# Kernel tuning notes

Hardware: AMD Instinct MI355X
Metric: run time of the kernel (lower is better)

## Reference

```python
import jax, jax.numpy as jnp
import numpy as np

B, N, D = 2, 2048, 768
H = 12
HD = D // H
HID = 4 * D
SCALE = HD ** -0.5
EPS = 1e-5


def layer_norm(x, g, b):
    mu = jnp.mean(x, axis=-1, keepdims=True)
    var = jnp.var(x, axis=-1, keepdims=True)
    return (x - mu) * jax.lax.rsqrt(var + EPS) * g + b


def setup_inputs() -> dict:
    key = jax.random.key(0)
    ks = jax.random.split(key, 12)
    s = 0.02
    return {
        "x": jax.random.normal(ks[0], (B, N, D), jnp.float32),
        "att_mask": jax.random.randint(ks[1], (B, N), 0, 2, jnp.int32),
        "ln1_g": jnp.ones((D,), jnp.float32),
        "ln1_b": jnp.zeros((D,), jnp.float32),
        "qkv_w": jax.random.normal(ks[2], (3 * D, D), jnp.float32) * s,
        "q_bias": jnp.zeros((D,), jnp.float32),
        "v_bias": jnp.zeros((D,), jnp.float32),
        "proj_w": jax.random.normal(ks[3], (D, D), jnp.float32) * s,
        "proj_b": jnp.zeros((D,), jnp.float32),
        "ln2_g": jnp.ones((D,), jnp.float32),
        "ln2_b": jnp.zeros((D,), jnp.float32),
        "fc1_w": jax.random.normal(ks[4], (HID, D), jnp.float32) * s,
        "fc1_b": jnp.zeros((HID,), jnp.float32),
        "fc2_w": jax.random.normal(ks[5], (D, HID), jnp.float32) * s,
        "fc2_b": jnp.zeros((D,), jnp.float32),
        "gamma_1": 0.1 * jnp.ones((D,), jnp.float32),
        "gamma_2": 0.1 * jnp.ones((D,), jnp.float32),
    }


def reference(x, att_mask, ln1_g, ln1_b, qkv_w, q_bias, v_bias, proj_w, proj_b,
              ln2_g, ln2_b, fc1_w, fc1_b, fc2_w, fc2_b, gamma_1, gamma_2):
    # --- attention branch ---
    h = layer_norm(x, ln1_g, ln1_b)
    qkv_bias = jnp.concatenate([q_bias, jnp.zeros_like(v_bias), v_bias])
    qkv = h @ qkv_w.T + qkv_bias                      # [B,N,3D]
    qkv = qkv.reshape(B, N, 3, H, HD).transpose(2, 0, 3, 1, 4)
    q, k, v = qkv[0], qkv[1], qkv[2]                  # [B,H,N,HD]
    logit = jnp.einsum('bhqd,bhkd->bhqk', q * SCALE, k)
    mask = att_mask[:, None, None, :]                 # key mask [B,1,1,N]
    logit = jnp.where(mask == 0, -jnp.inf, logit)
    attn = jax.nn.softmax(logit, axis=-1)
    o = jnp.einsum('bhqk,bhkd->bhqd', attn, v)
    o = o.transpose(0, 2, 1, 3).reshape(B, N, D)
    o = o @ proj_w.T + proj_b
    x = x + gamma_1 * o
    # --- mlp branch ---
    h2 = layer_norm(x, ln2_g, ln2_b)
    h2 = jax.nn.gelu(h2 @ fc1_w.T + fc1_b, approximate=False)
    h2 = h2 @ fc2_w.T + fc2_b
    return x + gamma_2 * h2
```

## Files before the change

kernel.cpp:

```cpp
#include <hip/hip_runtime.h>
#include <hip/hip_bf16.h>
#include <stdint.h>

typedef __bf16 bf16x8 __attribute__((ext_vector_type(8)));
typedef __bf16 bf16x2 __attribute__((ext_vector_type(2)));
typedef unsigned short u16x8 __attribute__((ext_vector_type(8)));
typedef float f32x4 __attribute__((ext_vector_type(4)));
typedef float f32x16 __attribute__((ext_vector_type(16)));
typedef uint32_t u32x4 __attribute__((ext_vector_type(4)));

#define DMODEL 768
#define NSEQ   2048
#define BATCH  2
#define NHEAD  12
#define HDIM   64
#define HIDDEN 3072
#define PROWS  (BATCH * NHEAD * NSEQ)
#define NZ     4
#define QSCALE 0.18033688011112042f
#define MCONST 16.0f
#define PMASKED 1.52587890625e-05f

__device__ __forceinline__ uint16_t f2bf(float f) {
  __bf16 h = (__bf16)f;
  return __builtin_bit_cast(uint16_t, h);
}
__device__ __forceinline__ float bf2f(uint16_t u) {
  uint32_t x = (uint32_t)u << 16;
  return __builtin_bit_cast(float, x);
}
__device__ __forceinline__ bf16x8 ldb8(const uint16_t* p) {
  return __builtin_bit_cast(bf16x8, *reinterpret_cast<const u16x8*>(p));
}

using as1_void = __attribute__((address_space(1))) const void;
using as3_void = __attribute__((address_space(3))) void;
__device__ __forceinline__ void gload16(const uint16_t* src, uint16_t* lds) {
  __builtin_amdgcn_global_load_lds((as1_void*)src, (as3_void*)lds, 16, 0, 0);
}
#define MEMFENCE asm volatile("" ::: "memory")

#define N_QKVW  (3 * DMODEL * DMODEL)
#define N_PROJW (DMODEL * DMODEL)
#define N_FC1W  (HIDDEN * DMODEL)
#define N_FC2W  (DMODEL * HIDDEN)
__global__ __launch_bounds__(256) void cvt4_kernel(const float* __restrict__ s0,
                                                   const float* __restrict__ s1,
                                                   const float* __restrict__ s2,
                                                   const float* __restrict__ s3,
                                                   uint16_t* __restrict__ d0,
                                                   uint16_t* __restrict__ d1,
                                                   uint16_t* __restrict__ d2,
                                                   uint16_t* __restrict__ d3) {
  int i4 = (blockIdx.x * 256 + threadIdx.x) * 4;
  const float* s;
  uint16_t* d;
  if (i4 < N_QKVW) { s = s0 + i4; d = d0 + i4; }
  else if (i4 < N_QKVW + N_PROJW) { int j = i4 - N_QKVW; s = s1 + j; d = d1 + j; }
  else if (i4 < N_QKVW + N_PROJW + N_FC1W) { int j = i4 - N_QKVW - N_PROJW; s = s2 + j; d = d2 + j; }
  else { int j = i4 - N_QKVW - N_PROJW - N_FC1W; s = s3 + j; d = d3 + j; }
  float4 v = *reinterpret_cast<const float4*>(s);
  ushort4 o;
  o.x = f2bf(v.x); o.y = f2bf(v.y); o.z = f2bf(v.z); o.w = f2bf(v.w);
  *reinterpret_cast<ushort4*>(d) = o;
}

__global__ __launch_bounds__(256) void bias_kernel(const float* __restrict__ qb,
                                                   const float* __restrict__ vb,
                                                   float* __restrict__ out) {
  int j = blockIdx.x * 256 + threadIdx.x;
  if (j < 3 * DMODEL) {
    float v = 0.f;
    if (j < DMODEL) v = qb[j];
    else if (j >= 2 * DMODEL) v = vb[j - 2 * DMODEL];
    out[j] = v;
  }
}

__global__ __launch_bounds__(256) void ln_kernel(const float* __restrict__ x,
                                                 const float* __restrict__ g,
                                                 const float* __restrict__ bt,
                                                 uint16_t* __restrict__ out) {
  const int row = blockIdx.x;
  const int t = threadIdx.x;
  const float* xr = x + (size_t)row * DMODEL;
  float v0 = xr[t], v1 = xr[t + 256], v2 = xr[t + 512];
  float s = v0 + v1 + v2;
  float q = v0 * v0 + v1 * v1 + v2 * v2;
  for (int off = 32; off >= 1; off >>= 1) {
    s += __shfl_xor(s, off);
    q += __shfl_xor(q, off);
  }
  __shared__ float ss[4], sq[4];
  int w = t >> 6;
  if ((t & 63) == 0) { ss[w] = s; sq[w] = q; }
  __syncthreads();
  s = ss[0] + ss[1] + ss[2] + ss[3];
  q = sq[0] + sq[1] + sq[2] + sq[3];
  const float mean = s * (1.0f / DMODEL);
  const float var = q * (1.0f / DMODEL) - mean * mean;
  const float rstd = rsqrtf(var + 1e-5f);
  uint16_t* orow = out + (size_t)row * DMODEL;
  orow[t]       = f2bf((v0 - mean) * rstd * g[t]       + bt[t]);
  orow[t + 256] = f2bf((v1 - mean) * rstd * g[t + 256] + bt[t + 256]);
  orow[t + 512] = f2bf((v2 - mean) * rstd * g[t + 512] + bt[t + 512]);
}

template <int MODE>
__global__ __launch_bounds__(256, 3) void gemm128(const uint16_t* __restrict__ A,
                                                  const uint16_t* __restrict__ W,
                                                  const float* __restrict__ bias,
                                                  void* __restrict__ outp,
                                                  uint16_t* __restrict__ km,
                                                  uint16_t* __restrict__ vt,
                                                  const int* __restrict__ amask,
                                                  int M, int N, int K) {
  __shared__ uint16_t As[2][128 * 32];
  __shared__ uint16_t Bs[2][128 * 32];
  const int tid = threadIdx.x;
  const int lane = tid & 63;
  const int w = tid >> 6;
  const int wr = w >> 1, wc = w & 1;
  const int row0 = blockIdx.y * 128;
  const int col0 = blockIdx.x * 128;
  const int lr = lane & 15;
  const int g = lane >> 4;

  const int o0 = w * 1024 + lane * 16;
  const int o1 = o0 + 4096;
  const int r0s = o0 >> 6, c0s = (o0 & 63) >> 1;
  const int r1s = o1 >> 6, c1s = (o1 & 63) >> 1;
  const int l0 = (w * 1024) >> 1;
  const int l1 = l0 + 2048;
  const uint16_t* Abase = A + (size_t)row0 * K;
  const uint16_t* Wbase = W + (size_t)col0 * K;

  auto stage = [&](int kt) {
    uint16_t* Ad = &As[kt & 1][0];
    uint16_t* Bd = &Bs[kt & 1][0];
    const int kk = kt * 32;
    gload16(Abase + (size_t)r0s * K + kk + c0s, Ad + l0);
    gload16(Abase + (size_t)r1s * K + kk + c1s, Ad + l1);
    gload16(Wbase + (size_t)r0s * K + kk + c0s, Bd + l0);
    gload16(Wbase + (size_t)r1s * K + kk + c1s, Bd + l1);
  };

  f32x4 acc[4][4] = {};
  const int nt = K >> 5;
  stage(0);
  for (int kt = 0; kt < nt; ++kt) {
    if (kt + 1 < nt) {
      stage(kt + 1);
      asm volatile("s_waitcnt vmcnt(4)" ::: "memory");
    } else {
      asm volatile("s_waitcnt vmcnt(0)" ::: "memory");
    }
    __builtin_amdgcn_s_barrier();
    MEMFENCE;
    const uint16_t* Ab = &As[kt & 1][0];
    const uint16_t* Bb = &Bs[kt & 1][0];
    bf16x8 a[4], b[4];
#pragma unroll
    for (int m = 0; m < 4; ++m) a[m] = ldb8(Ab + (wr * 64 + m * 16 + lr) * 32 + g * 8);
#pragma unroll
    for (int n = 0; n < 4; ++n) b[n] = ldb8(Bb + (wc * 64 + n * 16 + lr) * 32 + g * 8);
#pragma unroll
    for (int m = 0; m < 4; ++m)
#pragma unroll
      for (int n = 0; n < 4; ++n)
        acc[m][n] = __builtin_amdgcn_mfma_f32_16x16x32_bf16(a[m], b[n], acc[m][n], 0, 0, 0);
    MEMFENCE;
    __builtin_amdgcn_s_barrier();
  }

  if constexpr (MODE == 0) {
    const int sect = col0 / DMODEL;
    const int bb = row0 >> 11;
    const int* mrow = amask + bb * NSEQ;
#pragma unroll
    for (int m = 0; m < 4; ++m) {
      int row = row0 + wr * 64 + m * 16 + g * 4;
      int nn = row & 2047;
      int mk[4];
#pragma unroll
      for (int ri = 0; ri < 4; ++ri) mk[ri] = mrow[nn + ri];
#pragma unroll
      for (int n = 0; n < 4; ++n) {
        int col = col0 + wc * 64 + n * 16 + lr;
        float bv = bias[col];
        if (sect == 0) {
#pragma unroll
          for (int ri = 0; ri < 4; ++ri)
            ((uint16_t*)outp)[(size_t)(row + ri) * DMODEL + col] =
                f2bf((acc[m][n][ri] + bv) * QSCALE);
        } else if (sect == 1) {
          int kc = col - DMODEL;
#pragma unroll
          for (int ri = 0; ri < 4; ++ri)
            km[(size_t)(row + ri) * DMODEL + kc] =
                mk[ri] ? f2bf(acc[m][n][ri] + bv) : (uint16_t)0;
        } else {
          int vc = col - 2 * DMODEL;
          int hh2 = vc >> 6, dd = vc & 63;
          ushort4 sv;
          sv.x = mk[0] ? f2bf(acc[m][n][0] + bv) : (uint16_t)0;
          sv.y = mk[1] ? f2bf(acc[m][n][1] + bv) : (uint16_t)0;
          sv.z = mk[2] ? f2bf(acc[m][n][2] + bv) : (uint16_t)0;
          sv.w = mk[3] ? f2bf(acc[m][n][3] + bv) : (uint16_t)0;
          *reinterpret_cast<ushort4*>(
              vt + ((size_t)((bb * NHEAD + hh2) * 64 + dd)) * NSEQ + nn) = sv;
        }
      }
    }
  } else {
#pragma unroll
    for (int m = 0; m < 4; ++m) {
      int row = row0 + wr * 64 + m * 16 + g * 4;
#pragma unroll
      for (int n = 0; n < 4; ++n) {
        int col = col0 + wc * 64 + n * 16 + lr;
        float bv = bias[col];
#pragma unroll
        for (int ri = 0; ri < 4; ++ri) {
          float val = acc[m][n][ri] + bv;
          float ge = 0.5f * val * (1.0f + erff(val * 0.70710678118654752f));
          ((uint16_t*)outp)[(size_t)(row + ri) * N + col] = f2bf(ge);
        }
      }
    }
  }
}

__global__ __launch_bounds__(256, 3) void gemm64(const uint16_t* __restrict__ A,
                                                 const uint16_t* __restrict__ W,
                                                 const float* __restrict__ bias,
                                                 float* __restrict__ outp,
                                                 const float* __restrict__ resid,
                                                 const float* __restrict__ gamma,
                                                 int M, int N, int K) {
  __shared__ uint16_t As[2][64 * 64];
  __shared__ uint16_t Bs[2][64 * 64];
  const int tid = threadIdx.x;
  const int lane = tid & 63;
  const int w = tid >> 6;
  const int wr = w >> 1, wc = w & 1;
  const int row0 = blockIdx.y * 64;
  const int col0 = blockIdx.x * 64;
  const int lr = lane & 15;
  const int g = lane >> 4;

  const int srow = tid >> 3;
  const int schunk = tid & 7;
  const uint16_t* Abase = A + (size_t)row0 * K;
  const uint16_t* Wbase = W + (size_t)col0 * K;

  auto stage = [&](int kt) {
    uint16_t* Ad = &As[kt & 1][0];
    uint16_t* Bd = &Bs[kt & 1][0];
    const int kk = kt * 64;
#pragma unroll
    for (int i = 0; i < 2; ++i) {
      const int row = i * 32 + srow;
      const int sc = (schunk ^ (row & 7)) * 8;
      gload16(Abase + (size_t)row * K + kk + sc, Ad + i * 2048 + w * 512);
      gload16(Wbase + (size_t)row * K + kk + sc, Bd + i * 2048 + w * 512);
    }
  };

  f32x4 acc[2][2] = {};
  const int nt = K >> 6;
  stage(0);
  for (int kt = 0; kt < nt; ++kt) {
    if (kt + 1 < nt) {
      stage(kt + 1);
      asm volatile("s_waitcnt vmcnt(4)" ::: "memory");
    } else {
      asm volatile("s_waitcnt vmcnt(0)" ::: "memory");
    }
    __builtin_amdgcn_s_barrier();
    MEMFENCE;
    const uint16_t* Ab = &As[kt & 1][0];
    const uint16_t* Bb = &Bs[kt & 1][0];
#pragma unroll
    for (int kk = 0; kk < 2; ++kk) {
      bf16x8 a[2], bf[2];
#pragma unroll
      for (int m = 0; m < 2; ++m) {
        const int row = wr * 32 + m * 16 + lr;
        a[m] = ldb8(Ab + row * 64 + (((kk * 4 + g) ^ (row & 7)) * 8));
      }
#pragma unroll
      for (int n = 0; n < 2; ++n) {
        const int row = wc * 32 + n * 16 + lr;
        bf[n] = ldb8(Bb + row * 64 + (((kk * 4 + g) ^ (row & 7)) * 8));
      }
#pragma unroll
      for (int m = 0; m < 2; ++m)
#pragma unroll
        for (int n = 0; n < 2; ++n)
          acc[m][n] = __builtin_amdgcn_mfma_f32_16x16x32_bf16(a[m], bf[n], acc[m][n], 0, 0, 0);
    }
    MEMFENCE;
    __builtin_amdgcn_s_barrier();
  }

#pragma unroll
  for (int m = 0; m < 2; ++m) {
    int row = row0 + wr * 32 + m * 16 + g * 4;
#pragma unroll
    for (int n = 0; n < 2; ++n) {
      int col = col0 + wc * 32 + n * 16 + lr;
      float bv = bias[col];
      float gv = gamma[col];
#pragma unroll
      for (int ri = 0; ri < 4; ++ri) {
        float val = acc[m][n][ri] + bv;
        size_t idx = (size_t)(row + ri) * N + col;
        outp[idx] = resid[idx] + gv * val;
      }
    }
  }
}

__global__ __launch_bounds__(512, 4) void attn_kernel(const uint16_t* __restrict__ qb_,
                                                      const uint16_t* __restrict__ km,
                                                      const uint16_t* __restrict__ vt,
                                                      const int* __restrict__ mask,
                                                      uint16_t* __restrict__ po,
                                                      float* __restrict__ pml) {
  __shared__ uint16_t Kb[2][64 * 64];
  __shared__ uint16_t Vb[2][64 * 64];
  __shared__ unsigned long long mbits[8];
  const int tid = threadIdx.x;
  const int lane = tid & 63;
  const int w = tid >> 6;
  const int bh = blockIdx.x;
  const int b = bh / NHEAD, hd = bh % NHEAD;
  const int z = blockIdx.z;
  const int kbase = z * 512;
  const int q0 = blockIdx.y * 256 + w * 32;
  const int l31 = lane & 31;
  const int hh = lane >> 5;

  const int* mb = mask + b * NSEQ;
  {
    unsigned long long bm = __ballot(mb[kbase + w * 64 + lane] != 0);
    if (lane == 0) mbits[w] = bm;
  }

  bf16x8 qa[4];
  const uint16_t* qptr = qb_ + (size_t)(b * NSEQ + q0 + l31) * DMODEL + hd * HDIM + hh * 8;
#pragma unroll
  for (int dblk = 0; dblk < 4; ++dblk) qa[dblk] = ldb8(qptr + dblk * 16);

  const uint16_t* kmb = km + (size_t)b * NSEQ * DMODEL + hd * HDIM;
  const uint16_t* vtb = vt + (size_t)bh * HDIM * NSEQ;

  __syncthreads();

  const int srow = tid >> 3;
  const int sxor = ((tid & 7) ^ (srow & 7)) * 8;
  auto stage = [&](int t) {
    const int pb = t & 1;
    const int k0 = kbase + t * 64;
    gload16(kmb + (size_t)(k0 + srow) * DMODEL + sxor, &Kb[pb][w * 512]);
    gload16(vtb + (size_t)srow * NSEQ + k0 + sxor, &Vb[pb][w * 512]);
  };

  u16x8 ones_u;
#pragma unroll
  for (int e = 0; e < 8; ++e) ones_u[e] = 0x3F80;
  const bf16x8 ones = __builtin_bit_cast(bf16x8, ones_u);

  f32x16 oacc[2] = {};
  f32x16 lacc = {};

  stage(0);
  for (int t = 0; t < 8; ++t) {
    if (t + 1 < 8) {
      stage(t + 1);
      asm volatile("s_waitcnt vmcnt(2)" ::: "memory");
    } else {
      asm volatile("s_waitcnt vmcnt(0)" ::: "memory");
    }
    __builtin_amdgcn_s_barrier();
    MEMFENCE;
    const uint16_t* Kbp = &Kb[t & 1][0];
    const uint16_t* Vbp = &Vb[t & 1][0];

    f32x16 st[2];
    __builtin_amdgcn_s_setprio(1);
#pragma unroll
    for (int kblk = 0; kblk < 2; ++kblk) {
      f32x16 acc = {};
      const uint16_t* kr = Kbp + (kblk * 32 + l31) * 64;
#pragma unroll
      for (int dblk = 0; dblk < 4; ++dblk) {
        bf16x8 kf = ldb8(kr + ((dblk * 2 + hh) ^ (l31 & 7)) * 8);
        acc = __builtin_amdgcn_mfma_f32_32x32x16_bf16(kf, qa[dblk], acc, 0, 0, 0);
      }
      st[kblk] = acc;
    }
    __builtin_amdgcn_s_setprio(0);

    uint32_t pk[2][8];
#pragma unroll
    for (int kblk = 0; kblk < 2; ++kblk)
#pragma unroll
      for (int wn = 0; wn < 8; ++wn) {
        float e0 = exp2f(st[kblk][2 * wn] - MCONST);
        float e1 = exp2f(st[kblk][2 * wn + 1] - MCONST);
        bf16x2 pr = {(__bf16)e0, (__bf16)e1};
        pk[kblk][wn] = __builtin_bit_cast(uint32_t, pr);
      }

    bf16x8 af[4];
#pragma unroll
    for (int kb16 = 0; kb16 < 4; ++kb16) {
      const int kblk = kb16 >> 1;
      const int a4 = (kb16 & 1) * 4;
      uint32_t ow0 = hh ? pk[kblk][a4 + 2] : pk[kblk][a4 + 0];
      uint32_t ow1 = hh ? pk[kblk][a4 + 3] : pk[kblk][a4 + 1];
      uint32_t gv0 = hh ? pk[kblk][a4 + 0] : pk[kblk][a4 + 2];
      uint32_t gv1 = hh ? pk[kblk][a4 + 1] : pk[kblk][a4 + 3];
      uint32_t sw0 = (uint32_t)__shfl_xor((int)gv0, 32);
      uint32_t sw1 = (uint32_t)__shfl_xor((int)gv1, 32);
      u32x4 afu;
      afu[0] = hh ? sw0 : ow0;
      afu[1] = hh ? sw1 : ow1;
      afu[2] = hh ? ow0 : sw0;
      afu[3] = hh ? ow1 : sw1;
      af[kb16] = __builtin_bit_cast(bf16x8, afu);
    }

    __builtin_amdgcn_s_setprio(1);
#pragma unroll
    for (int dblk = 0; dblk < 2; ++dblk) {
      const uint16_t* vr = Vbp + (dblk * 32 + l31) * 64;
#pragma unroll
      for (int kb16 = 0; kb16 < 4; ++kb16) {
        bf16x8 vf = ldb8(vr + ((kb16 * 2 + hh) ^ (l31 & 7)) * 8);
        oacc[dblk] = __builtin_amdgcn_mfma_f32_32x32x16_bf16(af[kb16], vf, oacc[dblk], 0, 0, 0);
      }
    }
#pragma unroll
    for (int kb16 = 0; kb16 < 4; ++kb16)
      lacc = __builtin_amdgcn_mfma_f32_32x32x16_bf16(af[kb16], ones, lacc, 0, 0, 0);
    __builtin_amdgcn_s_setprio(0);
    MEMFENCE;
    __builtin_amdgcn_s_barrier();
  }

  int cnt = 0;
#pragma unroll
  for (int it = 0; it < 8; ++it) cnt += 64 - __popcll(mbits[it]);
  const float cntf = (float)cnt * PMASKED;

  uint16_t* ob = po + ((size_t)z * PROWS + (size_t)bh * NSEQ + q0) * 64;
#pragma unroll
  for (int r = 0; r < 16; ++r) {
    const int qrow = (r & 3) + 8 * (r >> 2) + 4 * hh;
#pragma unroll
    for (int dblk = 0; dblk < 2; ++dblk)
      ob[(size_t)qrow * 64 + dblk * 32 + l31] = f2bf(oacc[dblk][r]);
  }
  if (l31 == 0) {
#pragma unroll
    for (int r = 0; r < 16; ++r) {
      const int qrow = (r & 3) + 8 * (r >> 2) + 4 * hh;
      pml[(size_t)z * PROWS + (size_t)bh * NSEQ + q0 + qrow] = lacc[r] - cntf;
    }
  }
}

__global__ __launch_bounds__(256) void merge_kernel(const uint16_t* __restrict__ po,
                                                    const float* __restrict__ pml,
                                                    uint16_t* __restrict__ o) {
  int gid = blockIdx.x * 256 + threadIdx.x;
  int row = gid >> 3;
  int c0 = (gid & 7) * 8;
  float L = 0.f;
#pragma unroll
  for (int zz = 0; zz < NZ; ++zz) L += pml[(size_t)zz * PROWS + row];
  float inv = L > 0.f ? 1.f / L : 0.f;
  float sum[8] = {};
#pragma unroll
  for (int zz = 0; zz < NZ; ++zz) {
    u16x8 a = *reinterpret_cast<const u16x8*>(po + ((size_t)zz * PROWS + row) * 64 + c0);
#pragma unroll
    for (int e = 0; e < 8; ++e) sum[e] += bf2f(a[e]);
  }
  int bh = row >> 11, q = row & 2047;
  int bb = bh / NHEAD, hh = bh % NHEAD;
  uint16_t* op = o + ((size_t)(bb * NSEQ + q) * DMODEL + hh * HDIM + c0);
  u16x8 outv;
#pragma unroll
  for (int e = 0; e < 8; ++e) outv[e] = f2bf(sum[e] * inv);
  *reinterpret_cast<u16x8*>(op) = outv;
}

extern "C" void kernel_launch(void* const* d_in, const int* in_sizes, int n_in,
                              void* d_out, int out_size, void* d_ws, size_t ws_size,
                              hipStream_t stream) {
  const float* x      = (const float*)d_in[0];
  const int*   amask  = (const int*)d_in[1];
  const float* ln1_g  = (const float*)d_in[2];
  const float* ln1_b  = (const float*)d_in[3];
  const float* qkv_w  = (const float*)d_in[4];
  const float* q_bias = (const float*)d_in[5];
  const float* v_bias = (const float*)d_in[6];
  const float* proj_w = (const float*)d_in[7];
  const float* proj_b = (const float*)d_in[8];
  const float* ln2_g  = (const float*)d_in[9];
  const float* ln2_b  = (const float*)d_in[10];
  const float* fc1_w  = (const float*)d_in[11];
  const float* fc1_b  = (const float*)d_in[12];
  const float* fc2_w  = (const float*)d_in[13];
  const float* fc2_b  = (const float*)d_in[14];
  const float* g1     = (const float*)d_in[15];
  const float* g2     = (const float*)d_in[16];

  char* ws = (char*)d_ws;
  uint16_t* qkvw_bf  = (uint16_t*)(ws + 0);
  uint16_t* projw_bf = (uint16_t*)(ws + 3538944);
  uint16_t* fc1w_bf  = (uint16_t*)(ws + 4718592);
  uint16_t* fc2w_bf  = (uint16_t*)(ws + 9437184);
  float*    qkvbias  = (float*)(ws + 14155776);
  uint16_t* h_bf     = (uint16_t*)(ws + 14164992);
  uint16_t* q_bf     = (uint16_t*)(ws + 20456448);
  uint16_t* km       = (uint16_t*)(ws + 26747904);
  uint16_t* vt_bf    = (uint16_t*)(ws + 33039360);
  uint16_t* po       = (uint16_t*)(ws + 39330816);
  float*    pml      = (float*)(ws + 64496640);
  uint16_t* o_bf     = q_bf;
  float*    x1_f     = (float*)(ws + 26747904);
  uint16_t* fc1_bf   = (uint16_t*)(ws + 39330816);
  uint16_t* h2_bf    = h_bf;

  const int M = BATCH * NSEQ;

  cvt4_kernel<<<(N_QKVW + N_PROJW + N_FC1W + N_FC2W) / 1024, 256, 0, stream>>>(
      qkv_w, proj_w, fc1_w, fc2_w, qkvw_bf, projw_bf, fc1w_bf, fc2w_bf);
  bias_kernel<<<(3 * DMODEL + 255) / 256, 256, 0, stream>>>(q_bias, v_bias, qkvbias);

  ln_kernel<<<M, 256, 0, stream>>>(x, ln1_g, ln1_b, h_bf);
  gemm128<0><<<dim3((3 * DMODEL) / 128, M / 128), 256, 0, stream>>>(
      h_bf, qkvw_bf, qkvbias, q_bf, km, vt_bf, amask, M, 3 * DMODEL, DMODEL);
  attn_kernel<<<dim3(BATCH * NHEAD, NSEQ / 256, NZ), 512, 0, stream>>>(
      q_bf, km, vt_bf, amask, po, pml);
  merge_kernel<<<(PROWS * 8) / 256, 256, 0, stream>>>(po, pml, o_bf);
  gemm64<<<dim3(DMODEL / 64, M / 64), 256, 0, stream>>>(
      o_bf, projw_bf, proj_b, x1_f, x, g1, M, DMODEL, DMODEL);
  ln_kernel<<<M, 256, 0, stream>>>(x1_f, ln2_g, ln2_b, h2_bf);
  gemm128<2><<<dim3(HIDDEN / 128, M / 128), 256, 0, stream>>>(
      h2_bf, fc1w_bf, fc1_b, fc1_bf, nullptr, nullptr, nullptr, M, HIDDEN, DMODEL);
  gemm64<<<dim3(DMODEL / 64, M / 64), 256, 0, stream>>>(
      fc1_bf, fc2w_bf, fc2_b, (float*)d_out, x1_f, g2, M, DMODEL, HIDDEN);
}
```

Measured before the change: 190.2 us.

## Give each attention wave two query tiles and compute row sums with VALU

The attention block shrinks from 8 to 4 waves, and each wave now handles 64 query rows as two 32-row tiles. Each K and V fragment read from LDS then feeds two MFMAs, which halves LDS traffic per unit of work. The row sum of P was computed with a ones-vector MFMA and is now accumulated in registers with adds plus a cross-half shuffle, which removes 4 MFMAs per tile. In exchange each wave holds more accumulator registers, and there are fewer waves per block to hide latency.

```diff
diff --git a/kernel.cpp b/kernel.cpp
--- a/kernel.cpp
+++ b/kernel.cpp
@@ -322,7 +322,7 @@
   }
 }
 
-__global__ __launch_bounds__(512, 4) void attn_kernel(const uint16_t* __restrict__ qb_,
+__global__ __launch_bounds__(256, 2) void attn_kernel(const uint16_t* __restrict__ qb_,
                                                       const uint16_t* __restrict__ km,
                                                       const uint16_t* __restrict__ vt,
                                                       const int* __restrict__ mask,
@@ -338,20 +338,25 @@
   const int b = bh / NHEAD, hd = bh % NHEAD;
   const int z = blockIdx.z;
   const int kbase = z * 512;
-  const int q0 = blockIdx.y * 256 + w * 32;
+  const int q0 = blockIdx.y * 256 + w * 64;
   const int l31 = lane & 31;
   const int hh = lane >> 5;
 
   const int* mb = mask + b * NSEQ;
-  {
-    unsigned long long bm = __ballot(mb[kbase + w * 64 + lane] != 0);
-    if (lane == 0) mbits[w] = bm;
-  }
-
-  bf16x8 qa[4];
-  const uint16_t* qptr = qb_ + (size_t)(b * NSEQ + q0 + l31) * DMODEL + hd * HDIM + hh * 8;
-#pragma unroll
-  for (int dblk = 0; dblk < 4; ++dblk) qa[dblk] = ldb8(qptr + dblk * 16);
+#pragma unroll
+  for (int it = 0; it < 2; ++it) {
+    unsigned long long bm = __ballot(mb[kbase + it * 256 + tid] != 0);
+    if (lane == 0) mbits[it * 4 + w] = bm;
+  }
+
+  bf16x8 qa[2][4];
+#pragma unroll
+  for (int s = 0; s < 2; ++s) {
+    const uint16_t* qptr =
+        qb_ + (size_t)(b * NSEQ + q0 + s * 32 + l31) * DMODEL + hd * HDIM + hh * 8;
+#pragma unroll
+    for (int dblk = 0; dblk < 4; ++dblk) qa[s][dblk] = ldb8(qptr + dblk * 16);
+  }
 
   const uint16_t* kmb = km + (size_t)b * NSEQ * DMODEL + hd * HDIM;
   const uint16_t* vtb = vt + (size_t)bh * HDIM * NSEQ;
@@ -363,23 +368,22 @@
   auto stage = [&](int t) {
     const int pb = t & 1;
     const int k0 = kbase + t * 64;
-    gload16(kmb + (size_t)(k0 + srow) * DMODEL + sxor, &Kb[pb][w * 512]);
-    gload16(vtb + (size_t)srow * NSEQ + k0 + sxor, &Vb[pb][w * 512]);
+#pragma unroll
+    for (int i = 0; i < 2; ++i) {
+      const int row = i * 32 + srow;
+      gload16(kmb + (size_t)(k0 + row) * DMODEL + sxor, &Kb[pb][i * 2048 + w * 512]);
+      gload16(vtb + (size_t)row * NSEQ + k0 + sxor, &Vb[pb][i * 2048 + w * 512]);
+    }
   };
 
-  u16x8 ones_u;
-#pragma unroll
-  for (int e = 0; e < 8; ++e) ones_u[e] = 0x3F80;
-  const bf16x8 ones = __builtin_bit_cast(bf16x8, ones_u);
-
-  f32x16 oacc[2] = {};
-  f32x16 lacc = {};
+  f32x16 oacc[2][2] = {};
+  float lsum[2] = {0.f, 0.f};
 
   stage(0);
   for (int t = 0; t < 8; ++t) {
     if (t + 1 < 8) {
       stage(t + 1);
-      asm volatile("s_waitcnt vmcnt(2)" ::: "memory");
+      asm volatile("s_waitcnt vmcnt(4)" ::: "memory");
     } else {
       asm volatile("s_waitcnt vmcnt(0)" ::: "memory");
     }
@@ -388,49 +392,57 @@
     const uint16_t* Kbp = &Kb[t & 1][0];
     const uint16_t* Vbp = &Vb[t & 1][0];
 
-    f32x16 st[2];
+    f32x16 st[2][2];
     __builtin_amdgcn_s_setprio(1);
 #pragma unroll
     for (int kblk = 0; kblk < 2; ++kblk) {
-      f32x16 acc = {};
+      f32x16 a0 = {}, a1 = {};
       const uint16_t* kr = Kbp + (kblk * 32 + l31) * 64;
 #pragma unroll
       for (int dblk = 0; dblk < 4; ++dblk) {
         bf16x8 kf = ldb8(kr + ((dblk * 2 + hh) ^ (l31 & 7)) * 8);
-        acc = __builtin_amdgcn_mfma_f32_32x32x16_bf16(kf, qa[dblk], acc, 0, 0, 0);
-      }
-      st[kblk] = acc;
+        a0 = __builtin_amdgcn_mfma_f32_32x32x16_bf16(kf, qa[0][dblk], a0, 0, 0, 0);
+        a1 = __builtin_amdgcn_mfma_f32_32x32x16_bf16(kf, qa[1][dblk], a1, 0, 0, 0);
+      }
+      st[0][kblk] = a0;
+      st[1][kblk] = a1;
     }
     __builtin_amdgcn_s_setprio(0);
 
-    uint32_t pk[2][8];
-#pragma unroll
-    for (int kblk = 0; kblk < 2; ++kblk)
-#pragma unroll
-      for (int wn = 0; wn < 8; ++wn) {
-        float e0 = exp2f(st[kblk][2 * wn] - MCONST);
-        float e1 = exp2f(st[kblk][2 * wn + 1] - MCONST);
-        bf16x2 pr = {(__bf16)e0, (__bf16)e1};
-        pk[kblk][wn] = __builtin_bit_cast(uint32_t, pr);
-      }
-
-    bf16x8 af[4];
-#pragma unroll
-    for (int kb16 = 0; kb16 < 4; ++kb16) {
-      const int kblk = kb16 >> 1;
-      const int a4 = (kb16 & 1) * 4;
-      uint32_t ow0 = hh ? pk[kblk][a4 + 2] : pk[kblk][a4 + 0];
-      uint32_t ow1 = hh ? pk[kblk][a4 + 3] : pk[kblk][a4 + 1];
-      uint32_t gv0 = hh ? pk[kblk][a4 + 0] : pk[kblk][a4 + 2];
-      uint32_t gv1 = hh ? pk[kblk][a4 + 1] : pk[kblk][a4 + 3];
-      uint32_t sw0 = (uint32_t)__shfl_xor((int)gv0, 32);
-      uint32_t sw1 = (uint32_t)__shfl_xor((int)gv1, 32);
-      u32x4 afu;
-      afu[0] = hh ? sw0 : ow0;
-      afu[1] = hh ? sw1 : ow1;
-      afu[2] = hh ? ow0 : sw0;
-      afu[3] = hh ? ow1 : sw1;
-      af[kb16] = __builtin_bit_cast(bf16x8, afu);
+    bf16x8 af[2][4];
+#pragma unroll
+    for (int s = 0; s < 2; ++s) {
+      uint32_t pk[2][8];
+      float ls = 0.f;
+#pragma unroll
+      for (int kblk = 0; kblk < 2; ++kblk)
+#pragma unroll
+        for (int wn = 0; wn < 8; ++wn) {
+          float e0 = exp2f(st[s][kblk][2 * wn] - MCONST);
+          float e1 = exp2f(st[s][kblk][2 * wn + 1] - MCONST);
+          ls += e0 + e1;
+          bf16x2 pr = {(__bf16)e0, (__bf16)e1};
+          pk[kblk][wn] = __builtin_bit_cast(uint32_t, pr);
+        }
+      ls += __shfl_xor(ls, 32);
+      lsum[s] += ls;
+#pragma unroll
+      for (int kb16 = 0; kb16 < 4; ++kb16) {
+        const int kblk = kb16 >> 1;
+        const int a4 = (kb16 & 1) * 4;
+        uint32_t ow0 = hh ? pk[kblk][a4 + 2] : pk[kblk][a4 + 0];
+        uint32_t ow1 = hh ? pk[kblk][a4 + 3] : pk[kblk][a4 + 1];
+        uint32_t gv0 = hh ? pk[kblk][a4 + 0] : pk[kblk][a4 + 2];
+        uint32_t gv1 = hh ? pk[kblk][a4 + 1] : pk[kblk][a4 + 3];
+        uint32_t sw0 = (uint32_t)__shfl_xor((int)gv0, 32);
+        uint32_t sw1 = (uint32_t)__shfl_xor((int)gv1, 32);
+        u32x4 afu;
+        afu[0] = hh ? sw0 : ow0;
+        afu[1] = hh ? sw1 : ow1;
+        afu[2] = hh ? ow0 : sw0;
+        afu[3] = hh ? ow1 : sw1;
+        af[s][kb16] = __builtin_bit_cast(bf16x8, afu);
+      }
     }
 
     __builtin_amdgcn_s_setprio(1);
@@ -440,12 +452,10 @@
 #pragma unroll
       for (int kb16 = 0; kb16 < 4; ++kb16) {
         bf16x8 vf = ldb8(vr + ((kb16 * 2 + hh) ^ (l31 & 7)) * 8);
-        oacc[dblk] = __builtin_amdgcn_mfma_f32_32x32x16_bf16(af[kb16], vf, oacc[dblk], 0, 0, 0);
-      }
-    }
-#pragma unroll
-    for (int kb16 = 0; kb16 < 4; ++kb16)
-      lacc = __builtin_amdgcn_mfma_f32_32x32x16_bf16(af[kb16], ones, lacc, 0, 0, 0);
+        oacc[0][dblk] = __builtin_amdgcn_mfma_f32_32x32x16_bf16(af[0][kb16], vf, oacc[0][dblk], 0, 0, 0);
+        oacc[1][dblk] = __builtin_amdgcn_mfma_f32_32x32x16_bf16(af[1][kb16], vf, oacc[1][dblk], 0, 0, 0);
+      }
+    }
     __builtin_amdgcn_s_setprio(0);
     MEMFENCE;
     __builtin_amdgcn_s_barrier();
@@ -456,20 +466,18 @@
   for (int it = 0; it < 8; ++it) cnt += 64 - __popcll(mbits[it]);
   const float cntf = (float)cnt * PMASKED;
 
-  uint16_t* ob = po + ((size_t)z * PROWS + (size_t)bh * NSEQ + q0) * 64;
-#pragma unroll
-  for (int r = 0; r < 16; ++r) {
-    const int qrow = (r & 3) + 8 * (r >> 2) + 4 * hh;
-#pragma unroll
-    for (int dblk = 0; dblk < 2; ++dblk)
-      ob[(size_t)qrow * 64 + dblk * 32 + l31] = f2bf(oacc[dblk][r]);
-  }
-  if (l31 == 0) {
+#pragma unroll
+  for (int s = 0; s < 2; ++s) {
+    uint16_t* ob = po + ((size_t)z * PROWS + (size_t)bh * NSEQ + q0 + s * 32) * 64;
 #pragma unroll
     for (int r = 0; r < 16; ++r) {
       const int qrow = (r & 3) + 8 * (r >> 2) + 4 * hh;
-      pml[(size_t)z * PROWS + (size_t)bh * NSEQ + q0 + qrow] = lacc[r] - cntf;
-    }
+#pragma unroll
+      for (int dblk = 0; dblk < 2; ++dblk)
+        ob[(size_t)qrow * 64 + dblk * 32 + l31] = f2bf(oacc[s][dblk][r]);
+    }
+    if (hh == 0)
+      pml[(size_t)z * PROWS + (size_t)bh * NSEQ + q0 + s * 32 + l31] = lsum[s] - cntf;
   }
 }
 
@@ -546,7 +554,7 @@
   ln_kernel<<<M, 256, 0, stream>>>(x, ln1_g, ln1_b, h_bf);
   gemm128<0><<<dim3((3 * DMODEL) / 128, M / 128), 256, 0, stream>>>(
       h_bf, qkvw_bf, qkvbias, q_bf, km, vt_bf, amask, M, 3 * DMODEL, DMODEL);
-  attn_kernel<<<dim3(BATCH * NHEAD, NSEQ / 256, NZ), 512, 0, stream>>>(
+  attn_kernel<<<dim3(BATCH * NHEAD, NSEQ / 256, NZ), 256, 0, stream>>>(
       q_bf, km, vt_bf, amask, po, pml);
   merge_kernel<<<(PROWS * 8) / 256, 256, 0, stream>>>(po, pml, o_bf);
   gemm64<<<dim3(DMODEL / 64, M / 64), 256, 0, stream>>>(
```

After: 194.5 us. +2.3%, slower.
